# Performance work log

Hardware: AMD Instinct MI355X
Metric: run time of the kernel (lower is better)

## Reference

```python
import jax, jax.numpy as jnp
from jax import lax
import numpy as np

B, T, F = 64, 128, 16
H = 512
S = 2  # num_seg; SEG_DICT['2'] = [8, 6], seg_cumsum = [2, 10, 16]


def timestep_embedding(t, dim, max_period=10000.0):
    half = dim // 2
    freqs = jnp.exp(-jnp.log(max_period) * jnp.arange(half, dtype=jnp.float32) / half)
    args = t[:, None] * freqs  # [N, half]
    return jnp.concatenate([jnp.cos(args), jnp.sin(args)], axis=-1)  # [N, dim]


def setup_inputs() -> dict:
    key = jax.random.key(0)
    ks = jax.random.split(key, 16)
    sc = lambda *sh: 1.0 / np.sqrt(sh[-1])
    inp = {
        'x': jax.random.normal(ks[0], (B, T, F), dtype=jnp.float32),
        'lengths': jax.random.randint(ks[1], (B,), 1, T + 1),
        'h0': jax.random.uniform(ks[2], (B, H), dtype=jnp.float32),
        'c0': jax.random.uniform(ks[3], (B, H), dtype=jnp.float32),
        'W_is0': jax.random.normal(ks[4], (H, 8), dtype=jnp.float32) * sc(8),
        'b_is0': jax.random.normal(ks[5], (H,), dtype=jnp.float32) * 0.01,
        'W_is1': jax.random.normal(ks[6], (H, 6), dtype=jnp.float32) * sc(6),
        'b_is1': jax.random.normal(ks[7], (H,), dtype=jnp.float32) * 0.01,
        'W_ih': jax.random.normal(ks[8], (4 * H, 3 * H), dtype=jnp.float32) * sc(3 * H),
        'W_hh': jax.random.normal(ks[9], (4 * H, H), dtype=jnp.float32) * sc(H),
        'b_ih': jax.random.normal(ks[10], (4 * H,), dtype=jnp.float32) * 0.01,
        'b_hh': jax.random.normal(ks[11], (4 * H,), dtype=jnp.float32) * 0.01,
        'W_o': jax.random.normal(ks[12], (F - 2, S * H), dtype=jnp.float32) * sc(S * H),
        'b_o': jax.random.normal(ks[13], (F - 2,), dtype=jnp.float32) * 0.01,
    }
    return inp


def reference(x, lengths, h0, c0, W_is0, b_is0, W_is1, b_is1,
              W_ih, W_hh, b_ih, b_hh, W_o, b_o):
    b, t, f = x.shape
    h = h0.shape[1]
    xf = x.reshape(-1, f)  # [B*T, F]

    # timestep embeddings from the two time columns (learning_type='diff')
    tc = timestep_embedding(xf[:, 0], h)
    tp = timestep_embedding(xf[:, 1], h)
    t_emb = jnp.concatenate([tc, tp], axis=-1)  # [B*T, 2H]

    # per-segment input linears (segments = cols 2:10 and 10:16)
    e0 = xf[:, 2:10] @ W_is0.T + b_is0
    e1 = xf[:, 10:16] @ W_is1.T + b_is1
    e0 = jnp.concatenate([e0, t_emb], axis=-1)[:, None, :]  # [B*T, 1, 3H]
    e1 = jnp.concatenate([e1, t_emb], axis=-1)[:, None, :]
    # faithful to torch: concat on dim=1 then reshape(batch, num_seg, seq_len, -1)
    embs = jnp.concatenate([e0, e1], axis=1).reshape(b, S, t, 3 * h)

    def cell(carry, xt):
        hh, cc = carry
        gates = xt @ W_ih.T + b_ih + hh @ W_hh.T + b_hh
        i, fg, g, o = jnp.split(gates, 4, axis=-1)  # torch LSTMCell order i,f,g,o
        cc = jax.nn.sigmoid(fg) * cc + jax.nn.sigmoid(i) * jnp.tanh(g)
        hh = jax.nn.sigmoid(o) * jnp.tanh(cc)
        return (hh, cc), hh

    hs = []
    for s in range(S):  # shared cell weights across segments (same nn.LSTMCell object)
        xs = jnp.swapaxes(embs[:, s], 0, 1)  # [T, B, 3H]
        _, h_seq = lax.scan(cell, (h0, c0), xs)  # [T, B, H]
        hs.append(jnp.swapaxes(h_seq, 0, 1))  # [B, T, H]
    hidden_states = jnp.stack(hs, axis=-2)  # [B, T, S, H]; dropout rate 0 -> identity

    idx = lengths - 1  # final valid timestep per sequence
    hfin = hidden_states[jnp.arange(b), idx].reshape(b, S * h)  # [B, S*H]
    out = jax.nn.sigmoid(hfin @ W_o.T + b_o)  # mlp_o: Linear + Sigmoid
    return out
```

## Files before the change

### kernel.cpp

```cpp
#include <hip/hip_runtime.h>
#include <hip/hip_bf16.h>
#include <stdint.h>


typedef __attribute__((ext_vector_type(8))) short bf16x8_t;
typedef __attribute__((ext_vector_type(4))) float f32x4_t;

#define SENT 0xAAAAAAAAu

#define OFF_G      0u
#define OFF_HH     50331648u
#define OFF_WHH    67239936u
#define OFF_WMID   69337088u
#define OFF_WC0    73531392u
#define OFF_WC1    73596928u
#define OFF_BC     73662464u
#define OFF_HFIN   73678848u
#define OFF_GFLAG  73940992u

__device__ __forceinline__ float bf2f(uint16_t u){
  union { uint32_t i; float f; } v; v.i = ((uint32_t)u) << 16; return v.f;
}
__device__ __forceinline__ uint16_t f2b(float f){
  union { float f; uint32_t i; } v; v.f = f;
  uint32_t r = v.i + 0x7fffu + ((v.i >> 16) & 1u);
  return (uint16_t)(r >> 16);
}
__device__ __forceinline__ float sigm(float x){ return 1.0f/(1.0f + __expf(-x)); }
__device__ __forceinline__ float tanh_(float x){
  float xc = fminf(fmaxf(x, -15.f), 15.f);
  float t = __expf(2.f*xc);
  return (t - 1.f)/(t + 1.f);
}
__device__ __forceinline__ void gl_lds16(const void* g, void* l){
  __builtin_amdgcn_global_load_lds(
      (const __attribute__((address_space(1))) void*)g,
      (__attribute__((address_space(3))) void*)l, 16, 0, 0);
}

__global__ void prepAll(const float* __restrict__ W_ih, const float* __restrict__ W_hh,
                        const float* __restrict__ W_is0, const float* __restrict__ b_is0,
                        const float* __restrict__ W_is1, const float* __restrict__ b_is1,
                        const float* __restrict__ b_ih, const float* __restrict__ b_hh,
                        const float* __restrict__ h0,
                        uint16_t* __restrict__ whh_b, uint16_t* __restrict__ wmid_b,
                        float* __restrict__ wc0, float* __restrict__ wc1,
                        float* __restrict__ bc,
                        uint16_t* __restrict__ h_hist, uint32_t* __restrict__ gflag){
  const int bid = blockIdx.x, tid = threadIdx.x;
  if (bid < 2048){
    const int n = bid;
    __shared__ float wrow[512];
    __shared__ float red[16][17];
    wrow[tid]       = W_ih[(size_t)n*1536 + tid];
    wrow[tid + 256] = W_ih[(size_t)n*1536 + 256 + tid];
    for (int j = tid; j < 1024; j += 256)
      wmid_b[(size_t)n*1024 + j] = f2b(W_ih[(size_t)n*1536 + 512 + j]);
    for (int k = tid; k < 512; k += 256)
      whh_b[(size_t)n*512 + k] = f2b(W_hh[(size_t)n*512 + k]);
    __syncthreads();
    {
      const int d = tid >> 4, jp = tid & 15;
      float s = 0.f;
      const int kk0 = jp*32;
      if (d < 8){
        for (int k = kk0; k < kk0 + 32; ++k) s += wrow[k]*W_is0[k*8 + d];
      } else if (d < 14){
        int c = d - 8;
        for (int k = kk0; k < kk0 + 32; ++k) s += wrow[k]*W_is1[k*6 + c];
      } else if (d == 14){
        for (int k = kk0; k < kk0 + 32; ++k) s += wrow[k]*b_is0[k];
      } else {
        for (int k = kk0; k < kk0 + 32; ++k) s += wrow[k]*b_is1[k];
      }
      red[d][jp] = s;
    }
    __syncthreads();
    if (tid < 16){
      float tot = 0.f;
      #pragma unroll
      for (int i = 0; i < 16; ++i) tot += red[tid][i];
      if (tid < 8)        wc0[n*8 + tid] = tot;
      else if (tid < 14)  wc1[n*8 + (tid - 8)] = tot;
      else if (tid == 14) bc[n]        = b_ih[n] + b_hh[n] + tot;
      else                bc[2048 + n] = b_ih[n] + b_hh[n] + tot;
    } else if (tid == 16){
      wc1[n*8 + 6] = 0.f; wc1[n*8 + 7] = 0.f;
    }
  } else if (bid < 2176){
    int i = (bid - 2048)*256 + tid;
    uint32_t* hh = (uint32_t*)h_hist;
    int e    = i*2;
    int rrcg = e >> 9;
    int rr   = rrcg >> 4, cg = rrcg & 15;
    int rm   = e & 511;
    int row  = rm >> 5, u = rm & 31;
    int b    = (rr*16 + row) & 63;
    int unit = cg*32 + u;
    uint32_t lo = f2b(h0[(size_t)b*512 + unit]);
    uint32_t hi = f2b(h0[(size_t)b*512 + unit + 1]);
    uint32_t wd = lo | (hi << 16);
    if (wd == SENT) wd ^= 1u;
    hh[i] = wd;
    if (i < 1024) gflag[i] = 0u;
  } else {
    uint32_t* hh = (uint32_t*)h_hist;
    size_t w0 = 32768u + ((size_t)(bid - 2176)*256 + tid)*8;
    uint4 s4 = make_uint4(SENT, SENT, SENT, SENT);
    *(uint4*)&hh[w0]     = s4;
    *(uint4*)&hh[w0 + 4] = s4;
  }
}

__launch_bounds__(256)
__global__ void fusedk(const float* __restrict__ x, const float* __restrict__ c0,
                       const int* __restrict__ lengths,
                       const uint16_t* __restrict__ whh_b, const uint16_t* __restrict__ wmid,
                       const float* __restrict__ wc0, const float* __restrict__ wc1,
                       const float* __restrict__ bc,
                       uint16_t* __restrict__ G, uint16_t* __restrict__ h_hist,
                       uint32_t* __restrict__ gflag, float* __restrict__ hfin){
  __shared__ __align__(16) uint16_t smem_u[17664];
  const int tid = threadIdx.x;
  const int bid = blockIdx.x;
  const int w = tid >> 6, lane = tid & 63;
  const int q = lane >> 4, ln = lane & 15;

  if (bid >= 128){
    const int gb = bid - 128;
    const int idx = gb >> 4;
    const int mt = (idx & 1) ? (idx >> 1) : (32 + (idx >> 1));
    const int n0 = (gb & 15)*128;
    uint16_t* Al = smem_u;
    uint16_t* Bl = smem_u + 8192;
    const int wm = w >> 1, wn = w & 1;
    const int srow_l = lane >> 3, scol = (lane & 7)*8;

    float xs[4][2];
    #pragma unroll
    for (int i = 0; i < 4; ++i){
      int lrow = w*32 + i*8 + srow_l;
      int bA = lrow & 63, ntmA = mt*2 + (lrow >> 6);
      xs[i][0] = x[(size_t)(bA*128 + ntmA)*16 + 0];
      xs[i][1] = x[(size_t)(bA*128 + ntmA)*16 + 1];
    }

    f32x4_t acc[4][4];
    #pragma unroll
    for (int a = 0; a < 4; ++a)
      #pragma unroll
      for (int b2 = 0; b2 < 4; ++b2) acc[a][b2] = (f32x4_t){0.f,0.f,0.f,0.f};

    for (int kb = 0; kb < 16; ++kb){
      #pragma unroll
      for (int i = 0; i < 4; ++i){
        int row0 = w*32 + i*8;
        gl_lds16(wmid + (size_t)(n0 + row0 + srow_l)*1024 + kb*64 + scol, &Bl[row0*64]);
      }
      {
        uint16_t av[4][8];
        #pragma unroll
        for (int j = 0; j < 8; ++j){
          int col = kb*64 + scol + j;
          int sel = col >> 8;
          float f = __expf((float)(col & 255) * (-9.210340371976184f/256.f));
          #pragma unroll
          for (int i = 0; i < 4; ++i){
            float a = xs[i][sel >> 1]*f;
            float v = (sel & 1) ? __sinf(a) : __cosf(a);
            av[i][j] = f2b(v);
          }
        }
        #pragma unroll
        for (int i = 0; i < 4; ++i){
          int lrow = w*32 + i*8 + srow_l;
          *(uint4*)&Al[lrow*64 + scol] = *(uint4*)av[i];
        }
      }
      __syncthreads();
      #pragma unroll
      for (int kc = 0; kc < 2; ++kc){
        bf16x8_t af[4], bf[4];
        #pragma unroll
        for (int mt_i = 0; mt_i < 4; ++mt_i)
          af[mt_i] = *(const bf16x8_t*)&Al[(wm*64 + mt_i*16 + ln)*64 + kc*32 + q*8];
        #pragma unroll
        for (int nt = 0; nt < 4; ++nt)
          bf[nt] = *(const bf16x8_t*)&Bl[(wn*64 + nt*16 + ln)*64 + kc*32 + q*8];
        #pragma unroll
        for (int mt_i = 0; mt_i < 4; ++mt_i)
          #pragma unroll
          for (int nt = 0; nt < 4; ++nt)
            acc[mt_i][nt] = __builtin_amdgcn_mfma_f32_16x16x32_bf16(af[mt_i], bf[nt], acc[mt_i][nt], 0, 0, 0);
      }
      __syncthreads();
    }
    #pragma unroll
    for (int mt_i = 0; mt_i < 4; ++mt_i)
      #pragma unroll
      for (int nt = 0; nt < 4; ++nt)
        #pragma unroll
        for (int r = 0; r < 4; ++r){
          int Mr = wm*64 + mt_i*16 + q*4 + r;
          int Nc = wn*64 + nt*16 + ln;
          smem_u[Mr*128 + Nc] = f2b(acc[mt_i][nt][r]);
        }
    __syncthreads();
    {
      const int erow = tid >> 1, eh = tid & 1;
      const unsigned long long* lsrc = (const unsigned long long*)&smem_u[erow*128 + eh*64];
      unsigned long long* gdst = (unsigned long long*)
          (G + (size_t)(mt*128 + erow)*2048 + n0 + eh*64);
      #pragma unroll
      for (int i2 = 0; i2 < 16; ++i2)
        __hip_atomic_store(&gdst[i2], lsrc[i2], __ATOMIC_RELAXED, __HIP_MEMORY_SCOPE_AGENT);
    }
    __syncthreads();
    if (tid == 0)
      __hip_atomic_store(&gflag[mt*16 + (gb & 15)], 1u,
                         __ATOMIC_RELEASE, __HIP_MEMORY_SCOPE_AGENT);
    return;
  }

  asm volatile("s_setprio 3");
  #define HL(b,r,c) smem_u[(((b)*16 + (r))*552) + (c)]
  const int rr = bid & 7;
  const int g  = bid >> 3;
  const int k0 = g*32;
  const int sp = rr >> 2;
  const int u8 = ln & 7, gh = ln >> 3;
  const int unit = k0 + w*8 + u8;
  const int gl0 = gh*512 + unit;
  const int gl1 = (2 + gh)*512 + unit;
  const int LVL = 65536;

  bf16x8_t barr0[16], barr1[16];
  #pragma unroll
  for (int kc = 0; kc < 16; ++kc){
    barr0[kc] = *(const bf16x8_t*)(whh_b + (size_t)gl0*512 + kc*32 + q*8);
    barr1[kc] = *(const bf16x8_t*)(whh_b + (size_t)gl1*512 + kc*32 + q*8);
  }
  bf16x8_t e0f[2], e1f[2];
  #pragma unroll
  for (int nsI = 0; nsI < 2; ++nsI){
    bf16x8_t v0 = {0,0,0,0,0,0,0,0}, v1 = {0,0,0,0,0,0,0,0};
    if (q == 0){
      const float* wcs = nsI ? wc1 : wc0;
      #pragma unroll
      for (int jj = 0; jj < 8; ++jj){
        ((uint16_t*)&v0)[jj] = f2b(wcs[gl0*8 + jj]);
        ((uint16_t*)&v1)[jj] = f2b(wcs[gl1*8 + jj]);
      }
    }
    e0f[nsI] = v0; e1f[nsI] = v1;
  }
  float bc0v[2] = { bc[gl0], bc[2048 + gl0] };
  float bc1v[2] = { bc[gl1], bc[2048 + gl1] };

  int   bmr[4], lenr[4];
  float cst[4];
  #pragma unroll
  for (int r = 0; r < 4; ++r){
    int row = rr*16 + q*4 + r;
    bmr[r]  = row & 63;
    lenr[r] = lengths[bmr[r]];
    cst[r]  = c0[(size_t)bmr[r]*512 + unit];
  }

  const int prow = lane >> 2;
  const int pcol = (lane & 3)*8;
  const int xm = tid >> 3, xc = tid & 7;
  const int xb = (rr*16 + xm) & 63;
  const size_t stb = ((size_t)rr*8192 + g*512);

  for (int idx2 = tid; idx2 < 2*16*32; idx2 += 256)
    HL(idx2 >> 9, (idx2 >> 5) & 15, 520 + (idx2 & 31)) = 0;

  for (int t = 0; t < 128; ++t){
    const int qidx = sp*128 + t;
    const int ntm = qidx >> 1;
    const int ns  = qidx & 1;
    const int buf = t & 1;

    if ((t & 3) == 0){
      const int mt = qidx >> 2;
      const uint32_t* gf = gflag + mt*16 + (g >> 2);
      while (true){
        bool ok = true;
        #pragma unroll
        for (int j = 0; j < 4; ++j){
          uint32_t v = __hip_atomic_load(&gf[j*4], __ATOMIC_RELAXED, __HIP_MEMORY_SCOPE_AGENT);
          ok &= (v != 0u);
        }
        if (ok) break;
        __builtin_amdgcn_s_sleep(1);
      }
    }

    uint16_t g0r[4], g1r[4];
    #pragma unroll
    for (int r = 0; r < 4; ++r){
      size_t grow = (size_t)(ntm*64 + bmr[r])*2048;
      g0r[r] = G[grow + gl0];
      g1r[r] = G[grow + gl1];
    }
    float xv = 0.f;
    if (tid < 128){
      if (ns == 0)      xv = x[(size_t)(xb*128 + ntm)*16 + 2 + xc];
      else if (xc < 6)  xv = x[(size_t)(xb*128 + ntm)*16 + 10 + xc];
    }

    {
      const unsigned long long* lvl = (const unsigned long long*)h_hist
                                      + (((size_t)t*LVL + (size_t)rr*8192) >> 2);
      unsigned long long hv[4][2];
      while (true){
        bool ok = true;
        #pragma unroll
        for (int i = 0; i < 4; ++i){
          const unsigned long long* p = lvl + ((size_t)(w*4 + i)*128 + prow*8 + (pcol >> 2));
          hv[i][0] = __hip_atomic_load(&p[0], __ATOMIC_RELAXED, __HIP_MEMORY_SCOPE_AGENT);
          hv[i][1] = __hip_atomic_load(&p[1], __ATOMIC_RELAXED, __HIP_MEMORY_SCOPE_AGENT);
          ok &= ((uint32_t)hv[i][0] != SENT) & ((uint32_t)(hv[i][0] >> 32) != SENT)
              & ((uint32_t)hv[i][1] != SENT) & ((uint32_t)(hv[i][1] >> 32) != SENT);
        }
        if (__all(ok)) break;
        __builtin_amdgcn_s_sleep(1);
      }
      #pragma unroll
      for (int i = 0; i < 4; ++i){
        int reg = w*4 + i;
        *(unsigned long long*)&HL(buf, prow, reg*32 + pcol)     = hv[i][0];
        *(unsigned long long*)&HL(buf, prow, reg*32 + pcol + 4) = hv[i][1];
      }
    }
    if (tid < 128) HL(buf, xm, 512 + xc) = f2b(xv);
    __syncthreads();

    f32x4_t acc0, acc1;
    {
      float b0 = ns ? bc0v[1] : bc0v[0];
      float b1 = ns ? bc1v[1] : bc1v[0];
      #pragma unroll
      for (int r = 0; r < 4; ++r){ acc0[r] = bf2f(g0r[r]) + b0; acc1[r] = bf2f(g1r[r]) + b1; }
    }
    #pragma unroll
    for (int kc = 0; kc < 16; ++kc){
      bf16x8_t a = *(const bf16x8_t*)&HL(buf, ln, kc*32 + q*8);
      acc0 = __builtin_amdgcn_mfma_f32_16x16x32_bf16(a, barr0[kc], acc0, 0, 0, 0);
      acc1 = __builtin_amdgcn_mfma_f32_16x16x32_bf16(a, barr1[kc], acc1, 0, 0, 0);
    }
    {
      bf16x8_t a = *(const bf16x8_t*)&HL(buf, ln, 512 + q*8);
      acc0 = __builtin_amdgcn_mfma_f32_16x16x32_bf16(a, ns ? e0f[1] : e0f[0], acc0, 0, 0, 0);
      acc1 = __builtin_amdgcn_mfma_f32_16x16x32_bf16(a, ns ? e1f[1] : e1f[0], acc1, 0, 0, 0);
    }

    float pf[4], po[4];
    #pragma unroll
    for (int r = 0; r < 4; ++r){
      pf[r] = __shfl_xor(acc0[r], 8);
      po[r] = __shfl_xor(acc1[r], 8);
    }
    if (ln < 8){
      uint32_t hb[4]; float hF[4];
      #pragma unroll
      for (int r = 0; r < 4; ++r){
        float ig = acc0[r], fg = pf[r], gg = acc1[r], og = po[r];
        cst[r] = sigm(fg)*cst[r] + sigm(ig)*tanh_(gg);
        float h = sigm(og)*tanh_(cst[r]);
        hF[r] = h; hb[r] = (uint32_t)f2b(h);
      }
      #pragma unroll
      for (int r = 0; r < 4; ++r){
        uint32_t ph = (uint32_t)__shfl_xor((int)hb[r], 1);
        uint32_t packed = hb[r] | (ph << 16);
        if (packed == SENT) packed ^= 1u;
        uint32_t hi = (uint32_t)__shfl_xor((int)packed, 2);
        if ((ln & 3) == 0){
          unsigned long long v = (unsigned long long)packed | ((unsigned long long)hi << 32);
          unsigned long long* hp = (unsigned long long*)h_hist
              + (((size_t)(t+1)*LVL + stb + (size_t)(q*4 + r)*32 + w*8 + u8) >> 2);
          __hip_atomic_store(hp, v, __ATOMIC_RELAXED, __HIP_MEMORY_SCOPE_AGENT);
        }
        if (t == lenr[r] - 1)
          hfin[(size_t)bmr[r]*1024 + sp*512 + unit] = hF[r];
      }
    }
  }
  #undef HL
}

__global__ void outk(const float* __restrict__ hfin, const float* __restrict__ W_o,
                     const float* __restrict__ b_o, float* __restrict__ out){
  __shared__ float hl[1024];
  __shared__ float red[16][17];
  const int b = blockIdx.x, tid = threadIdx.x;
  #pragma unroll
  for (int i = 0; i < 4; ++i) hl[tid + i*256] = hfin[(size_t)b*1024 + tid + i*256];
  __syncthreads();
  const int o = tid >> 4, j0 = tid & 15;
  float s = 0.f;
  if (o < 14){
    for (int j = j0; j < 1024; j += 16) s += hl[j]*W_o[(size_t)o*1024 + j];
  }
  red[o][j0] = s;
  __syncthreads();
  if (tid < 14){
    float tot = b_o[tid];
    #pragma unroll
    for (int i = 0; i < 16; ++i) tot += red[tid][i];
    out[b*14 + tid] = 1.0f/(1.0f + __expf(-tot));
  }
}

extern "C" void kernel_launch(void* const* d_in, const int* in_sizes, int n_in,
                              void* d_out, int out_size, void* d_ws, size_t ws_size,
                              hipStream_t stream){
  const float* x     = (const float*)d_in[0];
  const int*   lens  = (const int*)  d_in[1];
  const float* h0    = (const float*)d_in[2];
  const float* c0    = (const float*)d_in[3];
  const float* W_is0 = (const float*)d_in[4];
  const float* b_is0 = (const float*)d_in[5];
  const float* W_is1 = (const float*)d_in[6];
  const float* b_is1 = (const float*)d_in[7];
  const float* W_ih  = (const float*)d_in[8];
  const float* W_hh  = (const float*)d_in[9];
  const float* b_ih  = (const float*)d_in[10];
  const float* b_hh  = (const float*)d_in[11];
  const float* W_o   = (const float*)d_in[12];
  const float* b_o   = (const float*)d_in[13];
  float* out = (float*)d_out;

  char* ws = (char*)d_ws;
  uint16_t* G      = (uint16_t*)(ws + OFF_G);
  uint16_t* h_hist = (uint16_t*)(ws + OFF_HH);
  uint16_t* whh_b  = (uint16_t*)(ws + OFF_WHH);
  uint16_t* wmid_b = (uint16_t*)(ws + OFF_WMID);
  float* wc0  = (float*)(ws + OFF_WC0);
  float* wc1  = (float*)(ws + OFF_WC1);
  float* bc   = (float*)(ws + OFF_BC);
  float* hfin = (float*)(ws + OFF_HFIN);
  uint32_t* gflag = (uint32_t*)(ws + OFF_GFLAG);

  hipLaunchKernelGGL(prepAll, dim3(4224), dim3(256), 0, stream,
                     W_ih, W_hh, W_is0, b_is0, W_is1, b_is1, b_ih, b_hh, h0,
                     whh_b, wmid_b, wc0, wc1, bc, h_hist, gflag);
  hipLaunchKernelGGL(fusedk, dim3(1152), dim3(256), 0, stream,
                     x, c0, lens, whh_b, wmid_b, wc0, wc1, bc,
                     G, h_hist, gflag, hfin);
  hipLaunchKernelGGL(outk, dim3(64), dim3(256), 0, stream, hfin, W_o, b_o, out);
}
```

Before: 571.6 us.

## Move weight prep into recurrent blocks and slim the init kernel

The prep kernel no longer converts W_hh to bf16 or computes the folded segment/bias weights. Each recurrent block now computes its own folded input weights and biases from W_ih and the segment linears, converts its W_hh rows to bf16 in registers, and writes the h0 history entries itself. The init kernel only fills sentinels, converts the W_ih middle columns with vectorized loads, and clears flags. This drops an intermediate buffer round trip and shrinks the prep kernel, but adds a serial 512-length dot-product loop at the start of each recurrent block and removes the s_setprio hint.

```diff
diff --git a/kernel.cpp b/kernel.cpp
--- a/kernel.cpp
+++ b/kernel.cpp
@@ -10,11 +10,7 @@
 
 #define OFF_G      0u
 #define OFF_HH     50331648u
-#define OFF_WHH    67239936u
 #define OFF_WMID   69337088u
-#define OFF_WC0    73531392u
-#define OFF_WC1    73596928u
-#define OFF_BC     73662464u
 #define OFF_HFIN   73678848u
 #define OFF_GFLAG  73940992u
 
@@ -38,86 +34,42 @@
       (__attribute__((address_space(3))) void*)l, 16, 0, 0);
 }
 
-__global__ void prepAll(const float* __restrict__ W_ih, const float* __restrict__ W_hh,
-                        const float* __restrict__ W_is0, const float* __restrict__ b_is0,
-                        const float* __restrict__ W_is1, const float* __restrict__ b_is1,
-                        const float* __restrict__ b_ih, const float* __restrict__ b_hh,
-                        const float* __restrict__ h0,
-                        uint16_t* __restrict__ whh_b, uint16_t* __restrict__ wmid_b,
-                        float* __restrict__ wc0, float* __restrict__ wc1,
-                        float* __restrict__ bc,
-                        uint16_t* __restrict__ h_hist, uint32_t* __restrict__ gflag){
+__global__ void initk(const float* __restrict__ W_ih, uint16_t* __restrict__ wmid_b,
+                      uint16_t* __restrict__ h_hist, uint32_t* __restrict__ gflag){
   const int bid = blockIdx.x, tid = threadIdx.x;
-  if (bid < 2048){
-    const int n = bid;
-    __shared__ float wrow[512];
-    __shared__ float red[16][17];
-    wrow[tid]       = W_ih[(size_t)n*1536 + tid];
-    wrow[tid + 256] = W_ih[(size_t)n*1536 + 256 + tid];
-    for (int j = tid; j < 1024; j += 256)
-      wmid_b[(size_t)n*1024 + j] = f2b(W_ih[(size_t)n*1536 + 512 + j]);
-    for (int k = tid; k < 512; k += 256)
-      whh_b[(size_t)n*512 + k] = f2b(W_hh[(size_t)n*512 + k]);
-    __syncthreads();
-    {
-      const int d = tid >> 4, jp = tid & 15;
-      float s = 0.f;
-      const int kk0 = jp*32;
-      if (d < 8){
-        for (int k = kk0; k < kk0 + 32; ++k) s += wrow[k]*W_is0[k*8 + d];
-      } else if (d < 14){
-        int c = d - 8;
-        for (int k = kk0; k < kk0 + 32; ++k) s += wrow[k]*W_is1[k*6 + c];
-      } else if (d == 14){
-        for (int k = kk0; k < kk0 + 32; ++k) s += wrow[k]*b_is0[k];
-      } else {
-        for (int k = kk0; k < kk0 + 32; ++k) s += wrow[k]*b_is1[k];
-      }
-      red[d][jp] = s;
-    }
-    __syncthreads();
-    if (tid < 16){
-      float tot = 0.f;
-      #pragma unroll
-      for (int i = 0; i < 16; ++i) tot += red[tid][i];
-      if (tid < 8)        wc0[n*8 + tid] = tot;
-      else if (tid < 14)  wc1[n*8 + (tid - 8)] = tot;
-      else if (tid == 14) bc[n]        = b_ih[n] + b_hh[n] + tot;
-      else                bc[2048 + n] = b_ih[n] + b_hh[n] + tot;
-    } else if (tid == 16){
-      wc1[n*8 + 6] = 0.f; wc1[n*8 + 7] = 0.f;
-    }
-  } else if (bid < 2176){
-    int i = (bid - 2048)*256 + tid;
+  if (bid < 2064){
     uint32_t* hh = (uint32_t*)h_hist;
-    int e    = i*2;
-    int rrcg = e >> 9;
-    int rr   = rrcg >> 4, cg = rrcg & 15;
-    int rm   = e & 511;
-    int row  = rm >> 5, u = rm & 31;
-    int b    = (rr*16 + row) & 63;
-    int unit = cg*32 + u;
-    uint32_t lo = f2b(h0[(size_t)b*512 + unit]);
-    uint32_t hi = f2b(h0[(size_t)b*512 + unit + 1]);
-    uint32_t wd = lo | (hi << 16);
-    if (wd == SENT) wd ^= 1u;
-    hh[i] = wd;
-    if (i < 1024) gflag[i] = 0u;
-  } else {
-    uint32_t* hh = (uint32_t*)h_hist;
-    size_t w0 = 32768u + ((size_t)(bid - 2176)*256 + tid)*8;
+    size_t w0 = ((size_t)bid*256 + tid)*8;
     uint4 s4 = make_uint4(SENT, SENT, SENT, SENT);
     *(uint4*)&hh[w0]     = s4;
     *(uint4*)&hh[w0 + 4] = s4;
+  } else if (bid < 2576){
+    int i = (bid - 2064)*256 + tid;
+    int n = i >> 6, c = (i & 63)*16;
+    const float* src = W_ih + (size_t)n*1536 + 512 + c;
+    uint16_t vv[16];
+    #pragma unroll
+    for (int j = 0; j < 16; j += 4){
+      float4 f4 = *(const float4*)&src[j];
+      vv[j] = f2b(f4.x); vv[j+1] = f2b(f4.y); vv[j+2] = f2b(f4.z); vv[j+3] = f2b(f4.w);
+    }
+    *(uint4*)&wmid_b[(size_t)n*1024 + c]     = *(uint4*)&vv[0];
+    *(uint4*)&wmid_b[(size_t)n*1024 + c + 8] = *(uint4*)&vv[8];
+  } else {
+    gflag[tid*4 + 0] = 0u; gflag[tid*4 + 1] = 0u;
+    gflag[tid*4 + 2] = 0u; gflag[tid*4 + 3] = 0u;
   }
 }
 
 __launch_bounds__(256)
 __global__ void fusedk(const float* __restrict__ x, const float* __restrict__ c0,
                        const int* __restrict__ lengths,
-                       const uint16_t* __restrict__ whh_b, const uint16_t* __restrict__ wmid,
-                       const float* __restrict__ wc0, const float* __restrict__ wc1,
-                       const float* __restrict__ bc,
+                       const float* __restrict__ W_ih, const float* __restrict__ W_hh,
+                       const float* __restrict__ W_is0, const float* __restrict__ b_is0,
+                       const float* __restrict__ W_is1, const float* __restrict__ b_is1,
+                       const float* __restrict__ b_ih, const float* __restrict__ b_hh,
+                       const float* __restrict__ h0,
+                       const uint16_t* __restrict__ wmid,
                        uint16_t* __restrict__ G, uint16_t* __restrict__ h_hist,
                        uint32_t* __restrict__ gflag, float* __restrict__ hfin){
   __shared__ __align__(16) uint16_t smem_u[17664];
@@ -222,7 +174,6 @@
     return;
   }
 
-  asm volatile("s_setprio 3");
   #define HL(b,r,c) smem_u[(((b)*16 + (r))*552) + (c)]
   const int rr = bid & 7;
   const int g  = bid >> 3;
@@ -234,28 +185,70 @@
   const int gl1 = (2 + gh)*512 + unit;
   const int LVL = 65536;
 
-  bf16x8_t barr0[16], barr1[16];
-  #pragma unroll
-  for (int kc = 0; kc < 16; ++kc){
-    barr0[kc] = *(const bf16x8_t*)(whh_b + (size_t)gl0*512 + kc*32 + q*8);
-    barr1[kc] = *(const bf16x8_t*)(whh_b + (size_t)gl1*512 + kc*32 + q*8);
-  }
+  float* scr = (float*)smem_u;
+  {
+    const int rowi = tid >> 1, half = tid & 1;
+    const int nrow = (rowi >> 5)*512 + k0 + (rowi & 31);
+    float a[8] = {0.f,0.f,0.f,0.f,0.f,0.f,0.f,0.f};
+    const float* wr = W_ih + (size_t)nrow*1536;
+    for (int k = 0; k < 512; k += 4){
+      float4 wv = *(const float4*)&wr[k];
+      float wk[4] = {wv.x, wv.y, wv.z, wv.w};
+      #pragma unroll
+      for (int kk = 0; kk < 4; ++kk){
+        float wvk = wk[kk]; int kg = k + kk;
+        if (half == 0){
+          #pragma unroll
+          for (int c = 0; c < 8; ++c) a[c] += wvk*W_is0[kg*8 + c];
+        } else {
+          #pragma unroll
+          for (int c = 0; c < 6; ++c) a[c] += wvk*W_is1[kg*6 + c];
+          a[6] += wvk*b_is0[kg];
+          a[7] += wvk*b_is1[kg];
+        }
+      }
+    }
+    #pragma unroll
+    for (int c = 0; c < 8; ++c) scr[rowi*16 + half*8 + c] = a[c];
+  }
+  __syncthreads();
+  const int lrow0 = gh*32 + (w*8 + u8);
+  const int lrow1 = (2 + gh)*32 + (w*8 + u8);
+  float bb0 = b_ih[gl0] + b_hh[gl0];
+  float bb1 = b_ih[gl1] + b_hh[gl1];
+  float bc0v[2] = { bb0 + scr[lrow0*16 + 14], bb0 + scr[lrow0*16 + 15] };
+  float bc1v[2] = { bb1 + scr[lrow1*16 + 14], bb1 + scr[lrow1*16 + 15] };
   bf16x8_t e0f[2], e1f[2];
   #pragma unroll
   for (int nsI = 0; nsI < 2; ++nsI){
     bf16x8_t v0 = {0,0,0,0,0,0,0,0}, v1 = {0,0,0,0,0,0,0,0};
     if (q == 0){
-      const float* wcs = nsI ? wc1 : wc0;
       #pragma unroll
       for (int jj = 0; jj < 8; ++jj){
-        ((uint16_t*)&v0)[jj] = f2b(wcs[gl0*8 + jj]);
-        ((uint16_t*)&v1)[jj] = f2b(wcs[gl1*8 + jj]);
+        float w0v = nsI ? ((jj < 6) ? scr[lrow0*16 + 8 + jj] : 0.f) : scr[lrow0*16 + jj];
+        float w1v = nsI ? ((jj < 6) ? scr[lrow1*16 + 8 + jj] : 0.f) : scr[lrow1*16 + jj];
+        ((uint16_t*)&v0)[jj] = f2b(w0v);
+        ((uint16_t*)&v1)[jj] = f2b(w1v);
       }
     }
     e0f[nsI] = v0; e1f[nsI] = v1;
   }
-  float bc0v[2] = { bc[gl0], bc[2048 + gl0] };
-  float bc1v[2] = { bc[gl1], bc[2048 + gl1] };
+  __syncthreads();
+
+  bf16x8_t barr0[16], barr1[16];
+  #pragma unroll
+  for (int kc = 0; kc < 16; ++kc){
+    const float* p0 = W_hh + (size_t)gl0*512 + kc*32 + q*8;
+    const float* p1 = W_hh + (size_t)gl1*512 + kc*32 + q*8;
+    float4 a0 = *(const float4*)p0, a1 = *(const float4*)(p0 + 4);
+    float4 b0 = *(const float4*)p1, b1 = *(const float4*)(p1 + 4);
+    uint16_t t0[8] = {f2b(a0.x),f2b(a0.y),f2b(a0.z),f2b(a0.w),
+                      f2b(a1.x),f2b(a1.y),f2b(a1.z),f2b(a1.w)};
+    uint16_t t1[8] = {f2b(b0.x),f2b(b0.y),f2b(b0.z),f2b(b0.w),
+                      f2b(b1.x),f2b(b1.y),f2b(b1.z),f2b(b1.w)};
+    barr0[kc] = *(bf16x8_t*)t0;
+    barr1[kc] = *(bf16x8_t*)t1;
+  }
 
   int   bmr[4], lenr[4];
   float cst[4];
@@ -273,6 +266,21 @@
   const int xb = (rr*16 + xm) & 63;
   const size_t stb = ((size_t)rr*8192 + g*512);
 
+  if (ln < 8 && (ln & 3) == 0){
+    #pragma unroll
+    for (int r = 0; r < 4; ++r){
+      float4 h4 = *(const float4*)&h0[(size_t)bmr[r]*512 + unit];
+      uint32_t p0 = (uint32_t)f2b(h4.x) | ((uint32_t)f2b(h4.y) << 16);
+      uint32_t p1 = (uint32_t)f2b(h4.z) | ((uint32_t)f2b(h4.w) << 16);
+      if (p0 == SENT) p0 ^= 1u;
+      if (p1 == SENT) p1 ^= 1u;
+      unsigned long long v = (unsigned long long)p0 | ((unsigned long long)p1 << 32);
+      unsigned long long* hp = (unsigned long long*)h_hist
+          + ((stb + (size_t)(q*4 + r)*32 + w*8 + u8) >> 2);
+      __hip_atomic_store(hp, v, __ATOMIC_RELAXED, __HIP_MEMORY_SCOPE_AGENT);
+    }
+  }
+
   for (int idx2 = tid; idx2 < 2*16*32; idx2 += 256)
     HL(idx2 >> 9, (idx2 >> 5) & 15, 520 + (idx2 & 31)) = 0;
 
@@ -290,7 +298,7 @@
         #pragma unroll
         for (int j = 0; j < 4; ++j){
           uint32_t v = __hip_atomic_load(&gf[j*4], __ATOMIC_RELAXED, __HIP_MEMORY_SCOPE_AGENT);
-          ok &= (v != 0u);
+          ok &= (v == 1u);
         }
         if (ok) break;
         __builtin_amdgcn_s_sleep(1);
@@ -436,19 +444,14 @@
   char* ws = (char*)d_ws;
   uint16_t* G      = (uint16_t*)(ws + OFF_G);
   uint16_t* h_hist = (uint16_t*)(ws + OFF_HH);
-  uint16_t* whh_b  = (uint16_t*)(ws + OFF_WHH);
   uint16_t* wmid_b = (uint16_t*)(ws + OFF_WMID);
-  float* wc0  = (float*)(ws + OFF_WC0);
-  float* wc1  = (float*)(ws + OFF_WC1);
-  float* bc   = (float*)(ws + OFF_BC);
   float* hfin = (float*)(ws + OFF_HFIN);
   uint32_t* gflag = (uint32_t*)(ws + OFF_GFLAG);
 
-  hipLaunchKernelGGL(prepAll, dim3(4224), dim3(256), 0, stream,
-                     W_ih, W_hh, W_is0, b_is0, W_is1, b_is1, b_ih, b_hh, h0,
-                     whh_b, wmid_b, wc0, wc1, bc, h_hist, gflag);
+  hipLaunchKernelGGL(initk, dim3(2577), dim3(256), 0, stream,
+                     W_ih, wmid_b, h_hist, gflag);
   hipLaunchKernelGGL(fusedk, dim3(1152), dim3(256), 0, stream,
-                     x, c0, lens, whh_b, wmid_b, wc0, wc1, bc,
-                     G, h_hist, gflag, hfin);
+                     x, c0, lens, W_ih, W_hh, W_is0, b_is0, W_is1, b_is1,
+                     b_ih, b_hh, h0, wmid_b, G, h_hist, gflag, hfin);
   hipLaunchKernelGGL(outk, dim3(64), dim3(256), 0, stream, hfin, W_o, b_o, out);
 }
```

New measurement: 631.4 us. +10.5%, slower.
